# Performance work log

Measured on AMD Instinct MI355X. Metric: run time of the kernel, lower is better.

## Reference

```python
import jax, jax.numpy as jnp
import numpy as np

WIN = (2, 6, 12)          # (vert, lat, lon) window size
HEADS = 6
DIM = 192
TYPES = 64                # type_of_windows = ceil(8/2)*ceil(96/6)
N = WIN[0] * WIN[1] * WIN[2]   # 144 patches per window


def _position_index():
    wz, wh, ww = WIN
    zi = np.arange(wz); zj = -np.arange(wz) * wz
    hi = np.arange(wh); hj = -np.arange(wh) * wh
    w = np.arange(ww)
    c1 = np.stack(np.meshgrid(zi, hi, w, indexing='ij')).reshape(3, -1)
    c2 = np.stack(np.meshgrid(zj, hj, w, indexing='ij')).reshape(3, -1)
    coords = (c1[:, :, None] - c2[:, None, :]).transpose(1, 2, 0)  # (N, N, 3)
    coords[:, :, 2] += ww - 1
    coords[:, :, 1] *= 2 * ww - 1
    coords[:, :, 0] *= (2 * ww - 1) * wh * wh
    return coords.sum(-1).reshape(-1)  # (N*N,) int

POS_IDX = jnp.asarray(_position_index())


def setup_inputs() -> dict:
    key = jax.random.key(0)
    ks = jax.random.split(key, 7)
    B = 960   # n_batch(1) * type_of_windows(64) * lon_windows(15)
    return {
        "x": jax.random.normal(ks[0], (B, N, DIM), jnp.float32),
        "mask": jax.random.normal(ks[1], (15, N, N), jnp.float32),
        "w_qkv": jax.random.normal(ks[2], (DIM, 3 * DIM), jnp.float32) * 0.02,
        "b_qkv": jax.random.normal(ks[3], (3 * DIM,), jnp.float32) * 0.02,
        "w_out": jax.random.normal(ks[4], (DIM, DIM), jnp.float32) * 0.02,
        "b_out": jax.random.normal(ks[5], (DIM,), jnp.float32) * 0.02,
        "bias_table": jax.random.normal(ks[6], (3312, TYPES, HEADS), jnp.float32) * 0.02,
    }


def reference(x, mask, w_qkv, b_qkv, w_out, b_out, bias_table):
    B = x.shape[0]
    hd = DIM // HEADS
    scale = hd ** -0.5

    qkv = (x @ w_qkv + b_qkv).reshape(B, N, 3, HEADS, hd)
    q, k, v = jnp.transpose(qkv, (2, 0, 3, 1, 4))      # each (B, H, N, hd)

    attn = jnp.einsum('bhnd,bhmd->bhnm', q * scale, k)  # (B, H, N, N)

    # gathered earth-specific absolute position bias: (TYPES, H, N, N)
    bias = bias_table[POS_IDX].reshape(N, N, TYPES, HEADS).transpose(2, 3, 0, 1)
    attn = (attn.reshape(-1, TYPES, HEADS, N, N) + bias[None]).reshape(B, HEADS, N, N)

    # additive mask over longitude-shifted windows
    n_w = mask.shape[0]
    attn = attn.reshape(B // n_w, n_w, HEADS, N, N) + mask[None, :, None]
    attn = attn.reshape(B, HEADS, N, N)

    attn = jax.nn.softmax(attn, axis=-1)               # dropout = identity (eval)

    out = jnp.einsum('bhnm,bhmd->bhnd', attn, v)       # (B, H, N, hd)
    out = out.transpose(0, 2, 1, 3).reshape(B, N, DIM)
    return out @ w_out + b_out
```

## Files before the change

kernel.cpp:

```cpp
#include <hip/hip_runtime.h>
#include <stdint.h>

typedef __bf16 bf16;
typedef __bf16 bf16x4 __attribute__((ext_vector_type(4)));
typedef __bf16 bf16x8 __attribute__((ext_vector_type(8)));
typedef float  f32x4  __attribute__((ext_vector_type(4)));

#define MFMA16(A, B, C) __builtin_amdgcn_mfma_f32_16x16x32_bf16((A), (B), (C), 0, 0, 0)

#define LOG2E 1.4426950408889634f


__global__ __launch_bounds__(256) void k_prep(const float* __restrict__ wqkv,
                                              const float* __restrict__ wout,
                                              bf16* __restrict__ wqkvt,
                                              bf16* __restrict__ woutt) {
    int i = blockIdx.x * 256 + threadIdx.x;
    if (i < 576 * 192) {
        int blk = i >> 9;
        int within = i & 511;
        int lane = within >> 3, j = within & 7;
        int strip = blk / 6, ks = blk - strip * 6;
        int col = strip * 16 + (lane & 15);
        int k = ks * 32 + (lane >> 4) * 8 + j;
        wqkvt[i] = (bf16)wqkv[k * 576 + col];
    } else {
        int jj = i - 576 * 192;
        int n = jj / 192, k = jj - n * 192;
        woutt[jj] = (bf16)wout[k * 192 + n];
    }
}

__global__ __launch_bounds__(256) void k_bias(const float* __restrict__ btab,
                                              bf16* __restrict__ bias) {
    __shared__ float tb[3312];
    const int th = blockIdx.x;
    for (int i = threadIdx.x; i < 3312; i += 256)
        tb[i] = btab[(size_t)i * 384 + th] * LOG2E;
    __syncthreads();
    bf16* op = bias + (size_t)th * 20736;
    for (int o = threadIdx.x; o < 20736; o += 256) {
        int nt = o / 2304, r1 = o - nt * 2304;
        int ct = r1 / 256,  r2 = r1 - ct * 256;
        int l15 = r2 >> 4,  gr = r2 & 15;
        int n = nt * 16 + l15, m = ct * 16 + gr;
        int zn = n / 72, rn = n - zn * 72, hn = rn / 12, wn = rn - hn * 12;
        int zm = m / 72, rm = m - zm * 72, hm = rm / 12, wm = rm - hm * 12;
        int idx = 828 * (zn + 2 * zm) + 23 * (hn + 6 * hm) + (wn - wm + 11);
        op[o] = (bf16)tb[idx];
    }
}

__global__ __launch_bounds__(256) void k_mswz(const float* __restrict__ mask,
                                              float* __restrict__ msw) {
    const int wm = blockIdx.x / 9;
    const int nt = blockIdx.x - wm * 9;
    const int tid = threadIdx.x;
    const int l15 = tid >> 4, gr = tid & 15;
    const float* src = mask + (size_t)wm * 20736 + (size_t)(nt * 16 + l15) * 144 + gr;
    float* dst = msw + (size_t)wm * 20736 + nt * 2304 + tid;
    #pragma unroll
    for (int ct = 0; ct < 9; ++ct)
        dst[ct * 256] = src[ct * 16];
}

__global__ __launch_bounds__(768, 3) void k_qkv(const float* __restrict__ x,
                                                const float* __restrict__ bqkv,
                                                const bf16* __restrict__ wtf,
                                                bf16* __restrict__ qb,
                                                bf16* __restrict__ kb,
                                                bf16* __restrict__ vtb) {
    __shared__ bf16 xs[96][200];
    const int tid = threadIdx.x;
    const int lane = tid & 63;
    const int w = tid >> 6;
    const int l15 = lane & 15;
    const int g = lane >> 4;
    const int c0 = w * 48;
    const int rowbase = blockIdx.x * 96;

    bf16x8 a[3][6];
    #pragma unroll
    for (int s = 0; s < 3; ++s)
        #pragma unroll
        for (int ks = 0; ks < 6; ++ks)
            a[s][ks] = *reinterpret_cast<const bf16x8*>(wtf + (size_t)(((w * 3 + s) * 6 + ks) * 512 + lane * 8));

    int hs[3], d0s[3], cgs[3];
    float scl[3];
    f32x4 bv[3];
    #pragma unroll
    for (int s = 0; s < 3; ++s) {
        int cbase = c0 + s * 16;
        int cg = cbase / 192;
        int rem = cbase - cg * 192;
        cgs[s] = cg;
        scl[s] = (cg == 0) ? 0.17677669529663687f * LOG2E : 1.0f;
        hs[s] = rem >> 5;
        d0s[s] = (rem & 31) + g * 4;
        bv[s] = *reinterpret_cast<const f32x4*>(bqkv + cbase + g * 4);
    }

    #pragma unroll
    for (int it = 0; it < 6; ++it) {
        int idx = tid + it * 768;
        int r = idx / 48, cp = idx - r * 48;
        f32x4 xa = *reinterpret_cast<const f32x4*>(x + (size_t)(rowbase + r) * 192 + cp * 4);
        bf16x4 v;
        v[0] = (bf16)xa[0]; v[1] = (bf16)xa[1]; v[2] = (bf16)xa[2]; v[3] = (bf16)xa[3];
        *reinterpret_cast<bf16x4*>(&xs[r][cp * 4]) = v;
    }
    __syncthreads();

    for (int sub = 0; sub < 6; ++sub) {
        const int row0 = rowbase + sub * 16;
        bf16x8 bfr[6];
        #pragma unroll
        for (int ks = 0; ks < 6; ++ks)
            bfr[ks] = *reinterpret_cast<const bf16x8*>(&xs[sub * 16 + l15][ks * 32 + g * 8]);
        f32x4 acc[3];
        #pragma unroll
        for (int s = 0; s < 3; ++s) acc[s] = (f32x4){0.f, 0.f, 0.f, 0.f};
        #pragma unroll
        for (int ks = 0; ks < 6; ++ks) {
            acc[0] = MFMA16(a[0][ks], bfr[ks], acc[0]);
            acc[1] = MFMA16(a[1][ks], bfr[ks], acc[1]);
            acc[2] = MFMA16(a[2][ks], bfr[ks], acc[2]);
        }
        const int bidx = row0 / 144;
        const int n = row0 - bidx * 144 + l15;
        #pragma unroll
        for (int s = 0; s < 3; ++s) {
            float v0 = (acc[s][0] + bv[s][0]) * scl[s];
            float v1 = (acc[s][1] + bv[s][1]) * scl[s];
            float v2 = (acc[s][2] + bv[s][2]) * scl[s];
            float v3 = (acc[s][3] + bv[s][3]) * scl[s];
            if (cgs[s] == 2) {
                bf16* dst = vtb + ((size_t)(bidx * 6 + hs[s]) * 32 + d0s[s]) * 144 + n;
                dst[0]   = (bf16)v0;
                dst[144] = (bf16)v1;
                dst[288] = (bf16)v2;
                dst[432] = (bf16)v3;
            } else {
                bf16x4 sv;
                sv[0] = (bf16)v0; sv[1] = (bf16)v1; sv[2] = (bf16)v2; sv[3] = (bf16)v3;
                bf16* base = (cgs[s] == 0) ? qb : kb;
                *reinterpret_cast<bf16x4*>(base + ((size_t)(bidx * 6 + hs[s]) * 144 + n) * 32 + d0s[s]) = sv;
            }
        }
    }
}

__global__ __launch_bounds__(192, 3) void k_attn(const bf16* __restrict__ qb,
                                                 const bf16* __restrict__ kb,
                                                 const bf16* __restrict__ vtb,
                                                 const float* __restrict__ msw,
                                                 const bf16* __restrict__ bias,
                                                 bf16* __restrict__ ob) {
    __shared__ bf16 pl[48][168];
    const int hb = blockIdx.x;
    const int b = hb / 6;
    const int h = hb - b * 6;
    const int t = b & 63;
    const int wm = b % 15;
    const int tid = threadIdx.x;
    const int lane = tid & 63;
    const int wv = tid >> 6;
    const int l15 = lane & 15;
    const int g = lane >> 4;

    const bf16* qp = qb + (size_t)hb * 4608;
    const bf16* kp = kb + (size_t)hb * 4608;
    const bf16* vp = vtb + (size_t)hb * 4608;

    bf16x8 kf[9];
    #pragma unroll
    for (int ct = 0; ct < 9; ++ct)
        kf[ct] = *reinterpret_cast<const bf16x8*>(kp + (size_t)(ct * 16 + l15) * 32 + g * 8);
    bf16x8 vf[10];
    #pragma unroll
    for (int mc = 0; mc < 5; ++mc) {
        vf[mc]     = *reinterpret_cast<const bf16x8*>(vp + (size_t)l15 * 144 + mc * 32 + g * 8);
        vf[5 + mc] = *reinterpret_cast<const bf16x8*>(vp + (size_t)(16 + l15) * 144 + mc * 32 + g * 8);
    }

    if (lane < 32) {
        bf16x8 z;
        #pragma unroll
        for (int i = 0; i < 8; ++i) z[i] = (bf16)0.f;
        *reinterpret_cast<bf16x8*>(&pl[wv * 16 + (lane >> 1)][144 + (lane & 1) * 8]) = z;
    }

    const float* mbase = msw + (size_t)wm * 20736 + l15 * 16 + g * 4;
    const bf16* bbase = bias + (size_t)(t * 6 + h) * 20736 + l15 * 16 + g * 4;

    for (int j = 0; j < 3; ++j) {
        const int n = j * 48 + wv * 16 + l15;
        const int nt = j * 3 + wv;

        bf16x8 bq = *reinterpret_cast<const bf16x8*>(qp + (size_t)n * 32 + g * 8);
        f32x4 s[9];
        #pragma unroll
        for (int ct = 0; ct < 9; ++ct) {
            f32x4 z = (f32x4){0.f, 0.f, 0.f, 0.f};
            s[ct] = MFMA16(kf[ct], bq, z);
        }

        const bf16* brow = bbase + nt * 2304;
        const float* mrow = mbase + nt * 2304;
        #pragma unroll
        for (int ct = 0; ct < 9; ++ct) {
            bf16x4 bvv = *reinterpret_cast<const bf16x4*>(brow + ct * 256);
            f32x4 mv = *reinterpret_cast<const f32x4*>(mrow + ct * 256);
            #pragma unroll
            for (int r = 0; r < 4; ++r)
                s[ct][r] = exp2f(fmaf(mv[r], LOG2E, s[ct][r] + (float)bvv[r]));
        }

        f32x4 sm4 = s[8];
        #pragma unroll
        for (int ct = 0; ct < 4; ++ct) {
            #pragma unroll
            for (int r = 0; r < 4; ++r)
                sm4[r] += s[ct][r] + s[ct + 4][r];
        }
        float rsum = (sm4[0] + sm4[1]) + (sm4[2] + sm4[3]);
        rsum += __shfl_xor(rsum, 16);
        rsum += __shfl_xor(rsum, 32);
        const float rinv = 1.0f / rsum;

        #pragma unroll
        for (int ct = 0; ct < 9; ++ct) {
            bf16x4 pv;
            #pragma unroll
            for (int r = 0; r < 4; ++r) pv[r] = (bf16)s[ct][r];
            *reinterpret_cast<bf16x4*>(&pl[wv * 16 + l15][ct * 16 + g * 4]) = pv;
        }
        __asm__ __volatile__("s_waitcnt lgkmcnt(0)" ::: "memory");

        f32x4 o0 = (f32x4){0.f, 0.f, 0.f, 0.f};
        f32x4 o1 = (f32x4){0.f, 0.f, 0.f, 0.f};
        #pragma unroll
        for (int mc = 0; mc < 5; ++mc) {
            bf16x8 pa = *reinterpret_cast<const bf16x8*>(&pl[wv * 16 + l15][mc * 32 + g * 8]);
            o0 = MFMA16(vf[mc], pa, o0);
            o1 = MFMA16(vf[5 + mc], pa, o1);
        }
        bf16* op = ob + (size_t)b * 27648 + (size_t)n * 192 + h * 32;
        bf16x4 s0, s1;
        #pragma unroll
        for (int r = 0; r < 4; ++r) { s0[r] = (bf16)(o0[r] * rinv); s1[r] = (bf16)(o1[r] * rinv); }
        *reinterpret_cast<bf16x4*>(op + g * 4)      = s0;
        *reinterpret_cast<bf16x4*>(op + 16 + g * 4) = s1;
    }
}

__global__ __launch_bounds__(768, 3) void k_out(const bf16* __restrict__ ob,
                                                const bf16* __restrict__ wt,
                                                const float* __restrict__ bout,
                                                float* __restrict__ out) {
    __shared__ bf16 os[96][200];
    __shared__ float ot[16][196];
    const int tid = threadIdx.x;
    const int lane = tid & 63;
    const int w = tid >> 6;
    const int l15 = lane & 15;
    const int g = lane >> 4;
    const int c0 = w * 16;
    const int rowbase = blockIdx.x * 96;

    bf16x8 a[6];
    #pragma unroll
    for (int ks = 0; ks < 6; ++ks)
        a[ks] = *reinterpret_cast<const bf16x8*>(wt + (size_t)(c0 + l15) * 192 + ks * 32 + g * 8);
    f32x4 bv = *reinterpret_cast<const f32x4*>(bout + c0 + g * 4);

    #pragma unroll
    for (int it = 0; it < 3; ++it) {
        int idx = tid + it * 768;
        int r = idx / 24, cp = idx - r * 24;
        bf16x8 v = *reinterpret_cast<const bf16x8*>(ob + (size_t)(rowbase + r) * 192 + cp * 8);
        *reinterpret_cast<bf16x8*>(&os[r][cp * 8]) = v;
    }
    __syncthreads();

    for (int sub = 0; sub < 6; ++sub) {
        bf16x8 bfr[6];
        #pragma unroll
        for (int ks = 0; ks < 6; ++ks)
            bfr[ks] = *reinterpret_cast<const bf16x8*>(&os[sub * 16 + l15][ks * 32 + g * 8]);
        f32x4 acc = (f32x4){0.f, 0.f, 0.f, 0.f};
        #pragma unroll
        for (int ks = 0; ks < 6; ++ks)
            acc = MFMA16(a[ks], bfr[ks], acc);
        __syncthreads();
        f32x4 sv;
        sv[0] = acc[0] + bv[0];
        sv[1] = acc[1] + bv[1];
        sv[2] = acc[2] + bv[2];
        sv[3] = acc[3] + bv[3];
        *reinterpret_cast<f32x4*>(&ot[l15][c0 + g * 4]) = sv;
        __syncthreads();
        int rr = tid / 48, c4 = tid - rr * 48;
        f32x4 vv = *reinterpret_cast<const f32x4*>(&ot[rr][c4 * 4]);
        *reinterpret_cast<f32x4*>(out + (size_t)(rowbase + sub * 16 + rr) * 192 + c4 * 4) = vv;
    }
}

extern "C" void kernel_launch(void* const* d_in, const int* in_sizes, int n_in,
                              void* d_out, int out_size, void* d_ws, size_t ws_size,
                              hipStream_t stream) {
    const float* x    = (const float*)d_in[0];
    const float* mask = (const float*)d_in[1];
    const float* wqkv = (const float*)d_in[2];
    const float* bqkv = (const float*)d_in[3];
    const float* wout = (const float*)d_in[4];
    const float* bout = (const float*)d_in[5];
    const float* btab = (const float*)d_in[6];
    float* out = (float*)d_out;

    char* ws = (char*)d_ws;
    bf16* wqkvt = (bf16*)(ws);
    bf16* woutt = (bf16*)(ws + 221184);
    bf16* bias  = (bf16*)(ws + 294912);
    bf16* obuf  = (bf16*)(ws + 16220160);
    bf16* qb    = (bf16*)(ws + 69304320);
    bf16* kb    = (bf16*)(ws + 122388480);
    bf16* vtb   = (bf16*)(ws + 175472640);
    float* msw  = (float*)(ws + 228556800);

    hipLaunchKernelGGL(k_prep, dim3(576),  dim3(256), 0, stream, wqkv, wout, wqkvt, woutt);
    hipLaunchKernelGGL(k_bias, dim3(384),  dim3(256), 0, stream, btab, bias);
    hipLaunchKernelGGL(k_mswz, dim3(135),  dim3(256), 0, stream, mask, msw);
    hipLaunchKernelGGL(k_qkv,  dim3(1440), dim3(768), 0, stream, x, bqkv, wqkvt, qb, kb, vtb);
    hipLaunchKernelGGL(k_attn, dim3(5760), dim3(192), 0, stream, qb, kb, vtb, msw, bias, obuf);
    hipLaunchKernelGGL(k_out,  dim3(1440), dim3(768), 0, stream, obuf, woutt, bout, out);
}
```

Measured before the change: 234.9 us.

## Stream weight fragments from global and batch three row tiles in QKV/out GEMMs

New measurement: 241.1 us. 2.7% more time.

```diff
diff --git a/kernel.cpp b/kernel.cpp
--- a/kernel.cpp
+++ b/kernel.cpp
@@ -26,8 +26,13 @@
         wqkvt[i] = (bf16)wqkv[k * 576 + col];
     } else {
         int jj = i - 576 * 192;
-        int n = jj / 192, k = jj - n * 192;
-        woutt[jj] = (bf16)wout[k * 192 + n];
+        int blk = jj >> 9;
+        int within = jj & 511;
+        int lane = within >> 3, j = within & 7;
+        int strip = blk / 6, ks = blk - strip * 6;
+        int col = strip * 16 + (lane & 15);
+        int k = ks * 32 + (lane >> 4) * 8 + j;
+        woutt[jj] = (bf16)wout[k * 192 + col];
     }
 }
 
@@ -79,13 +84,6 @@
     const int c0 = w * 48;
     const int rowbase = blockIdx.x * 96;
 
-    bf16x8 a[3][6];
-    #pragma unroll
-    for (int s = 0; s < 3; ++s)
-        #pragma unroll
-        for (int ks = 0; ks < 6; ++ks)
-            a[s][ks] = *reinterpret_cast<const bf16x8*>(wtf + (size_t)(((w * 3 + s) * 6 + ks) * 512 + lane * 8));
-
     int hs[3], d0s[3], cgs[3];
     float scl[3];
     f32x4 bv[3];
@@ -112,40 +110,52 @@
     }
     __syncthreads();
 
-    for (int sub = 0; sub < 6; ++sub) {
-        const int row0 = rowbase + sub * 16;
-        bf16x8 bfr[6];
-        #pragma unroll
-        for (int ks = 0; ks < 6; ++ks)
-            bfr[ks] = *reinterpret_cast<const bf16x8*>(&xs[sub * 16 + l15][ks * 32 + g * 8]);
-        f32x4 acc[3];
-        #pragma unroll
-        for (int s = 0; s < 3; ++s) acc[s] = (f32x4){0.f, 0.f, 0.f, 0.f};
+    for (int half = 0; half < 2; ++half) {
+        const int rbase = half * 48;
+        f32x4 acc[3][3];
+        #pragma unroll
+        for (int t = 0; t < 3; ++t)
+            #pragma unroll
+            for (int s = 0; s < 3; ++s)
+                acc[t][s] = (f32x4){0.f, 0.f, 0.f, 0.f};
+
         #pragma unroll
         for (int ks = 0; ks < 6; ++ks) {
-            acc[0] = MFMA16(a[0][ks], bfr[ks], acc[0]);
-            acc[1] = MFMA16(a[1][ks], bfr[ks], acc[1]);
-            acc[2] = MFMA16(a[2][ks], bfr[ks], acc[2]);
-        }
-        const int bidx = row0 / 144;
-        const int n = row0 - bidx * 144 + l15;
-        #pragma unroll
-        for (int s = 0; s < 3; ++s) {
-            float v0 = (acc[s][0] + bv[s][0]) * scl[s];
-            float v1 = (acc[s][1] + bv[s][1]) * scl[s];
-            float v2 = (acc[s][2] + bv[s][2]) * scl[s];
-            float v3 = (acc[s][3] + bv[s][3]) * scl[s];
-            if (cgs[s] == 2) {
-                bf16* dst = vtb + ((size_t)(bidx * 6 + hs[s]) * 32 + d0s[s]) * 144 + n;
-                dst[0]   = (bf16)v0;
-                dst[144] = (bf16)v1;
-                dst[288] = (bf16)v2;
-                dst[432] = (bf16)v3;
-            } else {
-                bf16x4 sv;
-                sv[0] = (bf16)v0; sv[1] = (bf16)v1; sv[2] = (bf16)v2; sv[3] = (bf16)v3;
-                bf16* base = (cgs[s] == 0) ? qb : kb;
-                *reinterpret_cast<bf16x4*>(base + ((size_t)(bidx * 6 + hs[s]) * 144 + n) * 32 + d0s[s]) = sv;
+            bf16x8 bfr0 = *reinterpret_cast<const bf16x8*>(&xs[rbase + 0  + l15][ks * 32 + g * 8]);
+            bf16x8 bfr1 = *reinterpret_cast<const bf16x8*>(&xs[rbase + 16 + l15][ks * 32 + g * 8]);
+            bf16x8 bfr2 = *reinterpret_cast<const bf16x8*>(&xs[rbase + 32 + l15][ks * 32 + g * 8]);
+            #pragma unroll
+            for (int s = 0; s < 3; ++s) {
+                bf16x8 aw = *reinterpret_cast<const bf16x8*>(wtf + (size_t)(((w * 3 + s) * 6 + ks) * 512 + lane * 8));
+                acc[0][s] = MFMA16(aw, bfr0, acc[0][s]);
+                acc[1][s] = MFMA16(aw, bfr1, acc[1][s]);
+                acc[2][s] = MFMA16(aw, bfr2, acc[2][s]);
+            }
+        }
+
+        #pragma unroll
+        for (int t = 0; t < 3; ++t) {
+            const int row0 = rowbase + rbase + t * 16;
+            const int bidx = row0 / 144;
+            const int n = row0 - bidx * 144 + l15;
+            #pragma unroll
+            for (int s = 0; s < 3; ++s) {
+                float v0 = (acc[t][s][0] + bv[s][0]) * scl[s];
+                float v1 = (acc[t][s][1] + bv[s][1]) * scl[s];
+                float v2 = (acc[t][s][2] + bv[s][2]) * scl[s];
+                float v3 = (acc[t][s][3] + bv[s][3]) * scl[s];
+                if (cgs[s] == 2) {
+                    bf16* dst = vtb + ((size_t)(bidx * 6 + hs[s]) * 32 + d0s[s]) * 144 + n;
+                    dst[0]   = (bf16)v0;
+                    dst[144] = (bf16)v1;
+                    dst[288] = (bf16)v2;
+                    dst[432] = (bf16)v3;
+                } else {
+                    bf16x4 sv;
+                    sv[0] = (bf16)v0; sv[1] = (bf16)v1; sv[2] = (bf16)v2; sv[3] = (bf16)v3;
+                    bf16* base = (cgs[s] == 0) ? qb : kb;
+                    *reinterpret_cast<bf16x4*>(base + ((size_t)(bidx * 6 + hs[s]) * 144 + n) * 32 + d0s[s]) = sv;
+                }
             }
         }
     }
@@ -256,11 +266,10 @@
 }
 
 __global__ __launch_bounds__(768, 3) void k_out(const bf16* __restrict__ ob,
-                                                const bf16* __restrict__ wt,
+                                                const bf16* __restrict__ wtf,
                                                 const float* __restrict__ bout,
                                                 float* __restrict__ out) {
     __shared__ bf16 os[96][200];
-    __shared__ float ot[16][196];
     const int tid = threadIdx.x;
     const int lane = tid & 63;
     const int w = tid >> 6;
@@ -269,10 +278,6 @@
     const int c0 = w * 16;
     const int rowbase = blockIdx.x * 96;
 
-    bf16x8 a[6];
-    #pragma unroll
-    for (int ks = 0; ks < 6; ++ks)
-        a[ks] = *reinterpret_cast<const bf16x8*>(wt + (size_t)(c0 + l15) * 192 + ks * 32 + g * 8);
     f32x4 bv = *reinterpret_cast<const f32x4*>(bout + c0 + g * 4);
 
     #pragma unroll
@@ -284,26 +289,31 @@
     }
     __syncthreads();
 
-    for (int sub = 0; sub < 6; ++sub) {
-        bf16x8 bfr[6];
-        #pragma unroll
-        for (int ks = 0; ks < 6; ++ks)
-            bfr[ks] = *reinterpret_cast<const bf16x8*>(&os[sub * 16 + l15][ks * 32 + g * 8]);
-        f32x4 acc = (f32x4){0.f, 0.f, 0.f, 0.f};
-        #pragma unroll
-        for (int ks = 0; ks < 6; ++ks)
-            acc = MFMA16(a[ks], bfr[ks], acc);
-        __syncthreads();
-        f32x4 sv;
-        sv[0] = acc[0] + bv[0];
-        sv[1] = acc[1] + bv[1];
-        sv[2] = acc[2] + bv[2];
-        sv[3] = acc[3] + bv[3];
-        *reinterpret_cast<f32x4*>(&ot[l15][c0 + g * 4]) = sv;
-        __syncthreads();
-        int rr = tid / 48, c4 = tid - rr * 48;
-        f32x4 vv = *reinterpret_cast<const f32x4*>(&ot[rr][c4 * 4]);
-        *reinterpret_cast<f32x4*>(out + (size_t)(rowbase + sub * 16 + rr) * 192 + c4 * 4) = vv;
+    for (int half = 0; half < 2; ++half) {
+        const int rbase = half * 48;
+        f32x4 acc[3];
+        #pragma unroll
+        for (int t = 0; t < 3; ++t) acc[t] = (f32x4){0.f, 0.f, 0.f, 0.f};
+        #pragma unroll
+        for (int ks = 0; ks < 6; ++ks) {
+            bf16x8 bfr0 = *reinterpret_cast<const bf16x8*>(&os[rbase + 0  + l15][ks * 32 + g * 8]);
+            bf16x8 bfr1 = *reinterpret_cast<const bf16x8*>(&os[rbase + 16 + l15][ks * 32 + g * 8]);
+            bf16x8 bfr2 = *reinterpret_cast<const bf16x8*>(&os[rbase + 32 + l15][ks * 32 + g * 8]);
+            bf16x8 aw = *reinterpret_cast<const bf16x8*>(wtf + (size_t)((w * 6 + ks) * 512 + lane * 8));
+            acc[0] = MFMA16(aw, bfr0, acc[0]);
+            acc[1] = MFMA16(aw, bfr1, acc[1]);
+            acc[2] = MFMA16(aw, bfr2, acc[2]);
+        }
+        #pragma unroll
+        for (int t = 0; t < 3; ++t) {
+            const int nn = rowbase + rbase + t * 16 + l15;
+            f32x4 v;
+            v[0] = acc[t][0] + bv[0];
+            v[1] = acc[t][1] + bv[1];
+            v[2] = acc[t][2] + bv[2];
+            v[3] = acc[t][3] + bv[3];
+            *reinterpret_cast<f32x4*>(out + (size_t)nn * 192 + c0 + g * 4) = v;
+        }
     }
 }
 
```
